# Performance work log

Measured on AMD Instinct MI355X. Metric: run time of the kernel, lower is better.

Reference implementation:

```python
import math
import jax, jax.numpy as jnp
import numpy as np

EMB = 1024
HEADS = 16
EXPAND = 2
HEAD_D = EMB // HEADS * EXPAND  # 128
N, S = 2, 2048


def setup_inputs() -> dict:
    key = jax.random.key(0)
    ks = jax.random.split(key, 10)
    lim = 1.0 / math.sqrt(EMB)  # nn.Linear default init range
    inp = {
        "query": jax.random.normal(ks[0], (N, S, EMB), dtype=jnp.float32),
        "key": jax.random.normal(ks[1], (N, S, EMB), dtype=jnp.float32),
        "value": jax.random.normal(ks[2], (N, S, EMB), dtype=jnp.float32),
        "mask": jax.random.randint(ks[3], (1, S, S), 0, 2, dtype=jnp.int32),
        "Wq": jax.random.uniform(ks[4], (EMB * EXPAND, EMB), jnp.float32, -lim, lim),
        "bq": jax.random.uniform(ks[5], (EMB * EXPAND,), jnp.float32, -lim, lim),
        "Wk": jax.random.uniform(ks[6], (EMB * EXPAND, EMB), jnp.float32, -lim, lim),
        "bk": jax.random.uniform(ks[7], (EMB * EXPAND,), jnp.float32, -lim, lim),
        "Wv": jax.random.uniform(ks[8], (EMB * EXPAND, EMB), jnp.float32, -lim, lim),
        "bv": jax.random.uniform(ks[9], (EMB * EXPAND,), jnp.float32, -lim, lim),
    }
    return inp


def _split_heads(x):
    # (N, S, H*D) -> (N, H, S, D)
    n, s, _ = x.shape
    return x.reshape(n, s, HEADS, HEAD_D).transpose(0, 2, 1, 3)


def reference(query, key, value, mask, Wq, bq, Wk, bk, Wv, bv):
    Q = _split_heads(jax.nn.relu(query @ Wq.T + bq))  # (N,H,S,D)
    K = _split_heads(jax.nn.relu(key @ Wk.T + bk))
    V = _split_heads(jax.nn.relu(value @ Wv.T + bv))
    scale = 1.0 / math.sqrt(HEAD_D)
    scores = jnp.einsum("nhqd,nhkd->nhqk", Q, K) * scale  # (N,H,S,S)
    scores = jnp.where(mask[None, :, :, :] == 0, jnp.float32(-1e7), scores)
    probs = jax.nn.softmax(scores, axis=-1)
    y = jnp.einsum("nhqk,nhkd->nhqd", probs, V)  # (N,H,S,D)
    return y.transpose(0, 2, 1, 3).reshape(query.shape[0], S, HEADS * HEAD_D)
```

## Files before the change

kernel.cpp:

```cpp
#include <hip/hip_runtime.h>

typedef __bf16 bf16;
typedef __bf16 bf16x8 __attribute__((ext_vector_type(8)));
typedef __bf16 bf16x4 __attribute__((ext_vector_type(4)));
typedef float f32x4 __attribute__((ext_vector_type(4)));

#define MFMA_BF16(A, B, C) __builtin_amdgcn_mfma_f32_16x16x32_bf16((A), (B), (C), 0, 0, 0)

#define EMB 1024
#define ODIM 2048
#define SEQ 2048
#define HEADS 16
#define HD 128

__global__ __launch_bounds__(256) void build_maskbits_k(const int* __restrict__ mask,
                                                        unsigned long long* __restrict__ mb) {
  int w = blockIdx.x * 256 + threadIdx.x;
  int q = w >> 5, c = w & 31;
  const int4* m4 = reinterpret_cast<const int4*>(mask + (size_t)q * SEQ + c * 64);
  unsigned long long bits = 0ull;
#pragma unroll
  for (int i = 0; i < 16; ++i) {
    int4 v = m4[i];
    if (v.x) bits |= 1ull << (i * 4 + 0);
    if (v.y) bits |= 1ull << (i * 4 + 1);
    if (v.z) bits |= 1ull << (i * 4 + 2);
    if (v.w) bits |= 1ull << (i * 4 + 3);
  }
  mb[w] = bits;
}

__global__ __launch_bounds__(256) void proj_gemm_k(const float* __restrict__ X,
                                                   const float* __restrict__ W,
                                                   const float* __restrict__ bias,
                                                   bf16* __restrict__ outN,
                                                   bf16* __restrict__ outT,
                                                   int vmode, float oscale) {
  __shared__ union {
    struct { bf16 A[128][40]; bf16 B[128][40]; } s;
    bf16 C[128][136];
  } sm;

  const int t = threadIdx.x;
  const int lane = t & 63;
  const int wid = t >> 6;
  const int wm = wid >> 1, wn = wid & 1;
  const int lr = lane & 15, lg = lane >> 4;
  const int m0 = blockIdx.y * 128;
  const int n0 = blockIdx.x * 128;
  const int sr = t >> 1, sh = (t & 1) * 16;

  const f32x4 fzero = {0.f, 0.f, 0.f, 0.f};
  f32x4 acc[4][4];
#pragma unroll
  for (int i = 0; i < 4; ++i)
#pragma unroll
    for (int j = 0; j < 4; ++j) acc[i][j] = fzero;

  const float* Xr = X + (size_t)(m0 + sr) * EMB + sh;
  const float* Wr = W + (size_t)(n0 + sr) * EMB + sh;

  float4 ar[4], br[4];
  {
    const float4* pa = reinterpret_cast<const float4*>(Xr);
    const float4* pb = reinterpret_cast<const float4*>(Wr);
#pragma unroll
    for (int i = 0; i < 4; ++i) { ar[i] = pa[i]; br[i] = pb[i]; }
  }

  for (int k0 = 0; k0 < EMB; k0 += 32) {
    {
      bf16x8 v0, v1, w0, w1;
      v0[0] = (bf16)ar[0].x; v0[1] = (bf16)ar[0].y; v0[2] = (bf16)ar[0].z; v0[3] = (bf16)ar[0].w;
      v0[4] = (bf16)ar[1].x; v0[5] = (bf16)ar[1].y; v0[6] = (bf16)ar[1].z; v0[7] = (bf16)ar[1].w;
      v1[0] = (bf16)ar[2].x; v1[1] = (bf16)ar[2].y; v1[2] = (bf16)ar[2].z; v1[3] = (bf16)ar[2].w;
      v1[4] = (bf16)ar[3].x; v1[5] = (bf16)ar[3].y; v1[6] = (bf16)ar[3].z; v1[7] = (bf16)ar[3].w;
      w0[0] = (bf16)br[0].x; w0[1] = (bf16)br[0].y; w0[2] = (bf16)br[0].z; w0[3] = (bf16)br[0].w;
      w0[4] = (bf16)br[1].x; w0[5] = (bf16)br[1].y; w0[6] = (bf16)br[1].z; w0[7] = (bf16)br[1].w;
      w1[0] = (bf16)br[2].x; w1[1] = (bf16)br[2].y; w1[2] = (bf16)br[2].z; w1[3] = (bf16)br[2].w;
      w1[4] = (bf16)br[3].x; w1[5] = (bf16)br[3].y; w1[6] = (bf16)br[3].z; w1[7] = (bf16)br[3].w;
      *(bf16x8*)&sm.s.A[sr][sh] = v0;
      *(bf16x8*)&sm.s.A[sr][sh + 8] = v1;
      *(bf16x8*)&sm.s.B[sr][sh] = w0;
      *(bf16x8*)&sm.s.B[sr][sh + 8] = w1;
    }
    __syncthreads();
    if (k0 + 32 < EMB) {
      const float4* pa = reinterpret_cast<const float4*>(Xr + k0 + 32);
      const float4* pb = reinterpret_cast<const float4*>(Wr + k0 + 32);
#pragma unroll
      for (int i = 0; i < 4; ++i) { ar[i] = pa[i]; br[i] = pb[i]; }
    }
    bf16x8 af[4], bfr[4];
#pragma unroll
    for (int i = 0; i < 4; ++i) af[i] = *(const bf16x8*)&sm.s.A[wm * 64 + i * 16 + lr][lg * 8];
#pragma unroll
    for (int i = 0; i < 4; ++i) bfr[i] = *(const bf16x8*)&sm.s.B[wn * 64 + i * 16 + lr][lg * 8];
#pragma unroll
    for (int mi = 0; mi < 4; ++mi)
#pragma unroll
      for (int ni = 0; ni < 4; ++ni)
        acc[mi][ni] = MFMA_BF16(af[mi], bfr[ni], acc[mi][ni]);
    __syncthreads();
  }

  float bv_[4];
#pragma unroll
  for (int ni = 0; ni < 4; ++ni) bv_[ni] = bias[n0 + wn * 64 + ni * 16 + lr];

  if (!vmode) {
#pragma unroll
    for (int mi = 0; mi < 4; ++mi)
#pragma unroll
      for (int ni = 0; ni < 4; ++ni)
#pragma unroll
        for (int j = 0; j < 4; ++j) {
          float v = fmaxf(acc[mi][ni][j] + bv_[ni], 0.f) * oscale;
          int row = m0 + wm * 64 + mi * 16 + lg * 4 + j;
          int col = n0 + wn * 64 + ni * 16 + lr;
          outN[(size_t)row * ODIM + col] = (bf16)v;
        }
  } else {
#pragma unroll
    for (int mi = 0; mi < 4; ++mi)
#pragma unroll
      for (int ni = 0; ni < 4; ++ni)
#pragma unroll
        for (int j = 0; j < 4; ++j) {
          float v = fmaxf(acc[mi][ni][j] + bv_[ni], 0.f) * oscale;
          int rit = wm * 64 + mi * 16 + lg * 4 + j;
          int cit = wn * 64 + ni * 16 + lr;
          sm.C[cit][rit] = (bf16)v;
        }
    __syncthreads();
    const int n = m0 >> 11;
    const int s0 = m0 & (SEQ - 1);
    const int h = blockIdx.x;
    bf16* base = outT + ((size_t)(n * HEADS + h) * HD) * SEQ + s0;
#pragma unroll
    for (int i = 0; i < 8; ++i) {
      int cid = i * 256 + t;
      int d = cid >> 4, c = cid & 15;
      *(bf16x8*)(base + (size_t)d * SEQ + c * 8) = *(const bf16x8*)&sm.C[d][c * 8];
    }
  }
}


__device__ __forceinline__ int kswz(int r, int c) {
  int b = (r << 8) | (c << 1);
  b ^= (r & 7) << 4;
  return b >> 1;
}
__device__ __forceinline__ int vswz(int d, int s) {
  int b = (d << 7) | (s << 1);
  b ^= (d & 7) << 4;
  return b >> 1;
}

__global__ __launch_bounds__(256, 2) void attn_k(const bf16* __restrict__ Qb,
                                                 const bf16* __restrict__ Kb,
                                                 const bf16* __restrict__ Vt,
                                                 const unsigned long long* __restrict__ mb,
                                                 float* __restrict__ out) {
  __shared__ bf16 Ks[64 * 128];
  __shared__ bf16 Vs[128 * 64];
  __shared__ bf16 Ps[4][32][72];

  const int t = threadIdx.x;
  const int lane = t & 63;
  const int w = t >> 6;
  const int lr = lane & 15, lg = lane >> 4;

  const int bid = blockIdx.x;
  const int swz = (bid & 7) * 64 + (bid >> 3);
  const int nh = swz >> 4;
  const int qt = swz & 15;
  const int n = nh >> 4, h = nh & 15;
  const int qrow = qt * 128 + w * 32;

  bf16x8 qf[2][4];
#pragma unroll
  for (int g = 0; g < 2; ++g) {
    const bf16* qp = Qb + (size_t)(n * SEQ + qrow + g * 16 + lr) * ODIM + h * HD + lg * 8;
#pragma unroll
    for (int ks = 0; ks < 4; ++ks) qf[g][ks] = *(const bf16x8*)(qp + ks * 32);
  }

  const bf16* Kg = Kb + (size_t)(n * SEQ) * ODIM + h * HD;
  const bf16* Vg = Vt + (size_t)nh * HD * SEQ;

  const int rK = t >> 4, cK = t & 15;
  const int dV = t >> 3, cV = t & 7;
  const bf16* kgp = Kg + (size_t)rK * ODIM + cK * 8;
  const bf16* vgp = Vg + (size_t)dV * SEQ + cV * 8;

  bf16x8 kreg[4], vreg[4];
#pragma unroll
  for (int i = 0; i < 4; ++i) kreg[i] = *(const bf16x8*)(kgp + (size_t)i * 16 * ODIM);
#pragma unroll
  for (int i = 0; i < 4; ++i) vreg[i] = *(const bf16x8*)(vgp + (size_t)i * 32 * SEQ);

  const f32x4 fzero = {0.f, 0.f, 0.f, 0.f};
  f32x4 oacc[2][8];
#pragma unroll
  for (int g = 0; g < 2; ++g)
#pragma unroll
    for (int i = 0; i < 8; ++i) oacc[g][i] = fzero;
  float mrun[2] = {-3.0e38f, -3.0e38f}, lrun[2] = {0.f, 0.f};

  const float L2E = 1.4426950408889634f;

  for (int kt = 0; kt < SEQ / 64; ++kt) {
#pragma unroll
    for (int i = 0; i < 4; ++i) *(bf16x8*)&Ks[kswz(rK + i * 16, cK * 8)] = kreg[i];
#pragma unroll
    for (int i = 0; i < 4; ++i) *(bf16x8*)&Vs[vswz(dV + i * 32, cV * 8)] = vreg[i];
    __syncthreads();

    if (kt + 1 < SEQ / 64) {
      const bf16* kn = kgp + (size_t)(kt + 1) * 64 * ODIM;
      const bf16* vn = vgp + (size_t)(kt + 1) * 64;
#pragma unroll
      for (int i = 0; i < 4; ++i) kreg[i] = *(const bf16x8*)(kn + (size_t)i * 16 * ODIM);
#pragma unroll
      for (int i = 0; i < 4; ++i) vreg[i] = *(const bf16x8*)(vn + (size_t)i * 32 * SEQ);
    }

    unsigned long long mw0 = mb[(size_t)(qrow + lr) * 32 + kt];
    unsigned long long mw1 = mb[(size_t)(qrow + 16 + lr) * 32 + kt];

    f32x4 sacc[2][4];
#pragma unroll
    for (int g = 0; g < 2; ++g)
#pragma unroll
      for (int f = 0; f < 4; ++f) sacc[g][f] = fzero;
#pragma unroll
    for (int f = 0; f < 4; ++f) {
#pragma unroll
      for (int ks = 0; ks < 4; ++ks) {
        bf16x8 kf = *(const bf16x8*)&Ks[kswz(f * 16 + lr, ks * 32 + lg * 8)];
        sacc[0][f] = MFMA_BF16(kf, qf[0][ks], sacc[0][f]);
        sacc[1][f] = MFMA_BF16(kf, qf[1][ks], sacc[1][f]);
      }
    }

    float mt[2] = {-3.0e38f, -3.0e38f};
#pragma unroll
    for (int f = 0; f < 4; ++f)
#pragma unroll
      for (int j = 0; j < 4; ++j) {
        int kk = f * 16 + lg * 4 + j;
        float x0 = ((mw0 >> kk) & 1ull) ? sacc[0][f][j] : -1.0e7f;
        float x1 = ((mw1 >> kk) & 1ull) ? sacc[1][f][j] : -1.0e7f;
        sacc[0][f][j] = x0;
        sacc[1][f][j] = x1;
        mt[0] = fmaxf(mt[0], x0);
        mt[1] = fmaxf(mt[1], x1);
      }
#pragma unroll
    for (int g = 0; g < 2; ++g) {
      mt[g] = fmaxf(mt[g], __shfl_xor(mt[g], 16));
      mt[g] = fmaxf(mt[g], __shfl_xor(mt[g], 32));
    }

    if (!__all((mt[0] <= mrun[0] + 8.0f) && (mt[1] <= mrun[1] + 8.0f))) {
#pragma unroll
      for (int g = 0; g < 2; ++g) {
        float mnew = fmaxf(mrun[g], mt[g]);
        float alpha = exp2f((mrun[g] - mnew) * L2E);
        mrun[g] = mnew;
        lrun[g] *= alpha;
#pragma unroll
        for (int df = 0; df < 8; ++df)
#pragma unroll
          for (int j = 0; j < 4; ++j) oacc[g][df][j] *= alpha;
      }
    }

    float psum[2] = {0.f, 0.f};
#pragma unroll
    for (int g = 0; g < 2; ++g)
#pragma unroll
      for (int f = 0; f < 4; ++f) {
        bf16x4 pw;
#pragma unroll
        for (int j = 0; j < 4; ++j) {
          float p = exp2f((sacc[g][f][j] - mrun[g]) * L2E);
          psum[g] += p;
          pw[j] = (bf16)p;
        }
        *(bf16x4*)&Ps[w][g * 16 + lr][f * 16 + lg * 4] = pw;
      }
#pragma unroll
    for (int g = 0; g < 2; ++g) {
      psum[g] += __shfl_xor(psum[g], 16);
      psum[g] += __shfl_xor(psum[g], 32);
      lrun[g] += psum[g];
    }

    bf16x8 pB[2][2];
#pragma unroll
    for (int g = 0; g < 2; ++g)
#pragma unroll
      for (int ks = 0; ks < 2; ++ks)
        pB[g][ks] = *(const bf16x8*)&Ps[w][g * 16 + lr][ks * 32 + lg * 8];

#pragma unroll
    for (int df = 0; df < 8; ++df) {
#pragma unroll
      for (int ks = 0; ks < 2; ++ks) {
        bf16x8 vf = *(const bf16x8*)&Vs[vswz(df * 16 + lr, ks * 32 + lg * 8)];
        oacc[0][df] = MFMA_BF16(vf, pB[0][ks], oacc[0][df]);
        oacc[1][df] = MFMA_BF16(vf, pB[1][ks], oacc[1][df]);
      }
    }
    __syncthreads();
  }

#pragma unroll
  for (int g = 0; g < 2; ++g) {
    float inv = 1.0f / lrun[g];
    float* obase = out + (size_t)(n * SEQ + qrow + g * 16 + lr) * ODIM + h * HD;
#pragma unroll
    for (int df = 0; df < 8; ++df) {
      f32x4 o;
#pragma unroll
      for (int j = 0; j < 4; ++j) o[j] = oacc[g][df][j] * inv;
      *(f32x4*)(obase + df * 16 + lg * 4) = o;
    }
  }
}

extern "C" void kernel_launch(void* const* d_in, const int* in_sizes, int n_in,
                              void* d_out, int out_size, void* d_ws, size_t ws_size,
                              hipStream_t stream) {
  const float* q   = (const float*)d_in[0];
  const float* k   = (const float*)d_in[1];
  const float* v   = (const float*)d_in[2];
  const int*  mask = (const int*)d_in[3];
  const float* Wq  = (const float*)d_in[4];
  const float* bq  = (const float*)d_in[5];
  const float* Wk  = (const float*)d_in[6];
  const float* bk  = (const float*)d_in[7];
  const float* Wv  = (const float*)d_in[8];
  const float* bv  = (const float*)d_in[9];
  float* out = (float*)d_out;

  char* ws = (char*)d_ws;
  const size_t PLANE = (size_t)4096 * 2048 * sizeof(bf16);
  bf16* Qb = (bf16*)ws;
  bf16* Kb = (bf16*)(ws + PLANE);
  bf16* Vt = (bf16*)(ws + 2 * PLANE);
  unsigned long long* mb = (unsigned long long*)(ws + 3 * PLANE);

  const float qscale = 0.08838834764831845f;

  build_maskbits_k<<<256, 256, 0, stream>>>(mask, mb);
  proj_gemm_k<<<dim3(16, 32), 256, 0, stream>>>(q, Wq, bq, Qb, nullptr, 0, qscale);
  proj_gemm_k<<<dim3(16, 32), 256, 0, stream>>>(k, Wk, bk, Kb, nullptr, 0, 1.0f);
  proj_gemm_k<<<dim3(16, 32), 256, 0, stream>>>(v, Wv, bv, nullptr, Vt, 1, 1.0f);
  attn_k<<<512, 256, 0, stream>>>(Qb, Kb, Vt, mb, out);
}
```

Baseline: 231.9 us.

## Compute softmax row sums via MFMA ones-row and fold log2e into Q scale

Appends a 16-row block to the V tile in shared memory. Its first row is all ones and the rest are zeros, so an extra MFMA column accumulates the softmax denominator and the per-tile shuffle reductions of psum go away. Folds log2(e) into the Q projection scale, which removes multiplies from the exp2 calls. Also seeds the score accumulators with the mask values (0 or -1e7) before the QK MFMAs, so no separate mask select pass is needed. The cost is one extra PV MFMA group per tile, a larger V shared buffer and more accumulator registers. The denominator is now summed from bf16-rounded probabilities, and the -1e7 mask constant now acts in the base-2 domain.

```diff
diff --git a/kernel.cpp b/kernel.cpp
--- a/kernel.cpp
+++ b/kernel.cpp
@@ -164,7 +164,7 @@
                                                  const unsigned long long* __restrict__ mb,
                                                  float* __restrict__ out) {
   __shared__ bf16 Ks[64 * 128];
-  __shared__ bf16 Vs[128 * 64];
+  __shared__ bf16 Vs[144 * 64];
   __shared__ bf16 Ps[4][32][72];
 
   const int t = threadIdx.x;
@@ -179,6 +179,14 @@
   const int n = nh >> 4, h = nh & 15;
   const int qrow = qt * 128 + w * 32;
 
+  {
+    int d = 128 + (t >> 4), s4 = (t & 15) * 4;
+    bf16 one = (bf16)1.0f, zero = (bf16)0.0f;
+    bf16x4 v = {zero, zero, zero, zero};
+    if (d == 128) { v[0] = one; v[1] = one; v[2] = one; v[3] = one; }
+    *(bf16x4*)&Vs[vswz(d, s4)] = v;
+  }
+
   bf16x8 qf[2][4];
 #pragma unroll
   for (int g = 0; g < 2; ++g) {
@@ -201,15 +209,12 @@
 #pragma unroll
   for (int i = 0; i < 4; ++i) vreg[i] = *(const bf16x8*)(vgp + (size_t)i * 32 * SEQ);
 
-  const f32x4 fzero = {0.f, 0.f, 0.f, 0.f};
-  f32x4 oacc[2][8];
+  f32x4 oacc[2][9];
 #pragma unroll
   for (int g = 0; g < 2; ++g)
 #pragma unroll
-    for (int i = 0; i < 8; ++i) oacc[g][i] = fzero;
-  float mrun[2] = {-3.0e38f, -3.0e38f}, lrun[2] = {0.f, 0.f};
-
-  const float L2E = 1.4426950408889634f;
+    for (int i = 0; i < 9; ++i) oacc[g][i] = {0.f, 0.f, 0.f, 0.f};
+  float mrun[2] = {-3.0e38f, -3.0e38f};
 
   for (int kt = 0; kt < SEQ / 64; ++kt) {
 #pragma unroll
@@ -232,9 +237,13 @@
 
     f32x4 sacc[2][4];
 #pragma unroll
-    for (int g = 0; g < 2; ++g)
-#pragma unroll
-      for (int f = 0; f < 4; ++f) sacc[g][f] = fzero;
+    for (int f = 0; f < 4; ++f)
+#pragma unroll
+      for (int j = 0; j < 4; ++j) {
+        int kk = f * 16 + lg * 4 + j;
+        sacc[0][f][j] = ((mw0 >> kk) & 1ull) ? 0.f : -1.0e7f;
+        sacc[1][f][j] = ((mw1 >> kk) & 1ull) ? 0.f : -1.0e7f;
+      }
 #pragma unroll
     for (int f = 0; f < 4; ++f) {
 #pragma unroll
@@ -247,19 +256,13 @@
 
     float mt[2] = {-3.0e38f, -3.0e38f};
 #pragma unroll
-    for (int f = 0; f < 4; ++f)
-#pragma unroll
-      for (int j = 0; j < 4; ++j) {
-        int kk = f * 16 + lg * 4 + j;
-        float x0 = ((mw0 >> kk) & 1ull) ? sacc[0][f][j] : -1.0e7f;
-        float x1 = ((mw1 >> kk) & 1ull) ? sacc[1][f][j] : -1.0e7f;
-        sacc[0][f][j] = x0;
-        sacc[1][f][j] = x1;
-        mt[0] = fmaxf(mt[0], x0);
-        mt[1] = fmaxf(mt[1], x1);
-      }
-#pragma unroll
     for (int g = 0; g < 2; ++g) {
+#pragma unroll
+      for (int f = 0; f < 4; ++f) {
+        float a = fmaxf(sacc[g][f][0], sacc[g][f][1]);
+        float b = fmaxf(sacc[g][f][2], sacc[g][f][3]);
+        mt[g] = fmaxf(mt[g], fmaxf(a, b));
+      }
       mt[g] = fmaxf(mt[g], __shfl_xor(mt[g], 16));
       mt[g] = fmaxf(mt[g], __shfl_xor(mt[g], 32));
     }
@@ -268,36 +271,24 @@
 #pragma unroll
       for (int g = 0; g < 2; ++g) {
         float mnew = fmaxf(mrun[g], mt[g]);
-        float alpha = exp2f((mrun[g] - mnew) * L2E);
+        float alpha = exp2f(mrun[g] - mnew);
         mrun[g] = mnew;
-        lrun[g] *= alpha;
-#pragma unroll
-        for (int df = 0; df < 8; ++df)
+#pragma unroll
+        for (int df = 0; df < 9; ++df)
 #pragma unroll
           for (int j = 0; j < 4; ++j) oacc[g][df][j] *= alpha;
       }
     }
 
-    float psum[2] = {0.f, 0.f};
 #pragma unroll
     for (int g = 0; g < 2; ++g)
 #pragma unroll
       for (int f = 0; f < 4; ++f) {
         bf16x4 pw;
 #pragma unroll
-        for (int j = 0; j < 4; ++j) {
-          float p = exp2f((sacc[g][f][j] - mrun[g]) * L2E);
-          psum[g] += p;
-          pw[j] = (bf16)p;
-        }
+        for (int j = 0; j < 4; ++j) pw[j] = (bf16)exp2f(sacc[g][f][j] - mrun[g]);
         *(bf16x4*)&Ps[w][g * 16 + lr][f * 16 + lg * 4] = pw;
       }
-#pragma unroll
-    for (int g = 0; g < 2; ++g) {
-      psum[g] += __shfl_xor(psum[g], 16);
-      psum[g] += __shfl_xor(psum[g], 32);
-      lrun[g] += psum[g];
-    }
 
     bf16x8 pB[2][2];
 #pragma unroll
@@ -307,7 +298,7 @@
         pB[g][ks] = *(const bf16x8*)&Ps[w][g * 16 + lr][ks * 32 + lg * 8];
 
 #pragma unroll
-    for (int df = 0; df < 8; ++df) {
+    for (int df = 0; df < 9; ++df) {
 #pragma unroll
       for (int ks = 0; ks < 2; ++ks) {
         bf16x8 vf = *(const bf16x8*)&Vs[vswz(df * 16 + lr, ks * 32 + lg * 8)];
@@ -320,7 +311,8 @@
 
 #pragma unroll
   for (int g = 0; g < 2; ++g) {
-    float inv = 1.0f / lrun[g];
+    float l = __shfl(oacc[g][8][0], lr);
+    float inv = 1.0f / l;
     float* obase = out + (size_t)(n * SEQ + qrow + g * 16 + lr) * ODIM + h * HD;
 #pragma unroll
     for (int df = 0; df < 8; ++df) {
@@ -354,7 +346,7 @@
   bf16* Vt = (bf16*)(ws + 2 * PLANE);
   unsigned long long* mb = (unsigned long long*)(ws + 3 * PLANE);
 
-  const float qscale = 0.08838834764831845f;
+  const float qscale = 0.08838834764831845f * 1.4426950408889634f;
 
   build_maskbits_k<<<256, 256, 0, stream>>>(mask, mb);
   proj_gemm_k<<<dim3(16, 32), 256, 0, stream>>>(q, Wq, bq, Qb, nullptr, 0, qscale);
```

After: 224.7 us. 3.1% less time.
